# Kernel optimization log

Measured on AMD Instinct MI355X. Metric: run time of the kernel, lower is better.

The kernel has to match this reference:

```python
import jax, jax.numpy as jnp
import numpy as np

N = 50000
E = 640000
H = 128

def setup_inputs() -> dict:
    key = jax.random.key(0)
    ks = jax.random.split(key, 12)
    def lin(kw, fan_in, fan_out):
        # torch nn.Linear default init: U(-1/sqrt(fan_in), 1/sqrt(fan_in))
        lim = 1.0 / np.sqrt(fan_in)
        return jax.random.uniform(kw, (fan_in, fan_out), jnp.float32, -lim, lim)
    def bias(kb, fan_in, fan_out):
        lim = 1.0 / np.sqrt(fan_in)
        return jax.random.uniform(kb, (fan_out,), jnp.float32, -lim, lim)
    return {
        "x": jax.random.normal(ks[0], (N, H), jnp.float32),
        "pos": jax.random.normal(ks[1], (N, 3), jnp.float32),
        "edge_index": jax.random.randint(ks[2], (2, E), 0, N, jnp.int64),
        "msg_w1": lin(ks[3], 2 * H + 1, H), "msg_b1": bias(ks[4], 2 * H + 1, H),
        "msg_w2": lin(ks[5], H, H),         "msg_b2": bias(ks[6], H, H),
        "upd_w1": lin(ks[7], 2 * H, H),     "upd_b1": bias(ks[8], 2 * H, H),
        "upd_w2": lin(ks[9], H, H),         "upd_b2": bias(ks[10], H, H),
    }

def reference(x, pos, edge_index, msg_w1, msg_b1, msg_w2, msg_b2,
              upd_w1, upd_b1, upd_w2, upd_b2):
    send, rec = edge_index[0], edge_index[1]
    # pairwise distance per edge: [E]
    dist = jnp.linalg.norm(pos[send] - pos[rec], axis=1)
    # per-edge state: [E, 2H+1]
    state = jnp.concatenate([x[send], x[rec], dist[:, None]], axis=1)
    # message MLP: Linear -> SiLU -> Linear -> SiLU
    h = jax.nn.silu(state @ msg_w1 + msg_b1)
    message = jax.nn.silu(h @ msg_w2 + msg_b2)  # [E, H]
    # scatter-add into receiving nodes: [N, H]
    aggr = jax.ops.segment_sum(message, rec, num_segments=x.shape[0])
    # update MLP: Linear -> SiLU -> Linear
    u = jax.nn.silu(jnp.concatenate([x, aggr], axis=1) @ upd_w1 + upd_b1)
    update = u @ upd_w2 + upd_b2
    return update
```

## Files before the change

kernel.cpp:

```cpp
#include <hip/hip_runtime.h>
#include <math.h>

#define H 128

typedef unsigned short u16;
typedef unsigned int u32;
typedef __attribute__((ext_vector_type(4))) u32 u32x4;
typedef __attribute__((ext_vector_type(8))) __bf16 bf16x8;
typedef __attribute__((ext_vector_type(4))) float f32x4;
typedef __attribute__((ext_vector_type(16))) float f32x16;

union Frag { u32x4 u; bf16x8 b; };

__device__ __forceinline__ u32 pack2(float lo, float hi) {
    union { __bf16 b[2]; u32 u; } v;
    v.b[0] = (__bf16)lo; v.b[1] = (__bf16)hi;
    return v.u;
}
__device__ __forceinline__ float bflo(u32 w) {
    union { u32 i; float f; } v; v.i = w << 16; return v.f;
}
__device__ __forceinline__ float bfhi(u32 w) {
    union { u32 i; float f; } v; v.i = w & 0xffff0000u; return v.f;
}
__device__ __forceinline__ float silu(float v) {
    float e = __expf(-v);
    return v * __builtin_amdgcn_rcpf(1.0f + e);
}
__device__ __forceinline__ bf16x8 f8frag(float4 lo, float4 hi) {
    Frag f;
    f.u = (u32x4){pack2(lo.x, lo.y), pack2(lo.z, lo.w),
                  pack2(hi.x, hi.y), pack2(hi.z, hi.w)};
    return f.b;
}
__device__ __forceinline__ f32x16 mfma(bf16x8 a, bf16x8 b, f32x16 c) {
    return __builtin_amdgcn_mfma_f32_32x32x16_bf16(a, b, c, 0, 0, 0);
}
__device__ __forceinline__ f32x4 mfma16(bf16x8 a, bf16x8 b, f32x4 c) {
    return __builtin_amdgcn_mfma_f32_16x16x32_bf16(a, b, c, 0, 0, 0);
}
#define DPP_RADD(v, ctrl) \
    (v) += __int_as_float(__builtin_amdgcn_update_dpp(0, __float_as_int(v), (ctrl), 0xf, 0xf, 1))

__global__ void prep_kernel(const float* __restrict__ mw1, const float* __restrict__ mb1,
                            const float* __restrict__ mw2, const float* __restrict__ mb2,
                            const float* __restrict__ uw1, const float* __restrict__ ub1,
                            const float* __restrict__ uw2, const float* __restrict__ ub2,
                            u32* __restrict__ ws) {
    int t = blockIdx.x * blockDim.x + threadIdx.x;
    if (t >= 15936) return;
    if (t >= 15872) {
        int i = t - 15872;
        ws[63488 + i] = pack2(mw1[256 * H + 2 * i], mw1[256 * H + 2 * i + 1]);
        return;
    }
    if (t >= 13312) {
        int slot = t - 13312;
        int lane = slot & 63, fb = slot >> 6;
        int kb = fb >> 3, mt = fb & 7;
        int m = mt * 16 + (lane & 15);
        int quad = lane >> 4;
        u32 out[4];
        #pragma unroll
        for (int p = 0; p < 4; ++p) {
            float v[2];
            #pragma unroll
            for (int h = 0; h < 2; ++h) {
                int k = kb * 32 + quad * 8 + p * 2 + h;
                float val = 0.0f;
                if (k < 128)       val = mw2[(size_t)k * H + m];
                else if (k == 128) val = mb2[m];
                v[h] = val;
            }
            out[p] = pack2(v[0], v[1]);
        }
        u32* dst = ws + 53248 + (size_t)slot * 4;
        dst[0] = out[0]; dst[1] = out[1]; dst[2] = out[2]; dst[3] = out[3];
        return;
    }
    const float *W, *s0, *s1;
    int nK, slot, base;
    if (t < 4352)       { W = mw1; s0 = mw1 + 256 * H; s1 = mb1; nK = 256; slot = t;         base = 0;     }
    else if (t < 6656)  { W = mw2; s0 = mb2; s1 = nullptr;       nK = 128; slot = t - 4352;  base = 17408; }
    else if (t < 11008) { W = uw1; s0 = ub1; s1 = nullptr;       nK = 256; slot = t - 6656;  base = 26624; }
    else                { W = uw2; s0 = ub2; s1 = nullptr;       nK = 128; slot = t - 11008; base = 44032; }
    int lane = slot & 63, fb = slot >> 6;
    int ct, kb;
    if (nK == 256) { ct = fb / 17; kb = fb % 17; }
    else           { ct = fb / 9;  kb = fb % 9;  }
    int m = ct * 32 + (lane & 31);
    int q = lane >> 5;
    u32 out[4];
    #pragma unroll
    for (int p = 0; p < 4; ++p) {
        float v[2];
        #pragma unroll
        for (int h = 0; h < 2; ++h) {
            int k = kb * 16 + q * 8 + p * 2 + h;
            float val = 0.0f;
            if (k < nK)            val = W[(size_t)k * H + m];
            else if (k == nK)      val = s0 ? s0[m] : 0.0f;
            else if (k == nK + 1)  val = s1 ? s1[m] : 0.0f;
            v[h] = val;
        }
        out[p] = pack2(v[0], v[1]);
    }
    u32* dst = ws + base + (size_t)slot * 4;
    dst[0] = out[0]; dst[1] = out[1]; dst[2] = out[2]; dst[3] = out[3];
}

__global__ __launch_bounds__(256, 2) void pq_gemm(
    const float* __restrict__ x, const u32* __restrict__ mw1s,
    void* __restrict__ outp, int kbBase, int withBias, int packP, int N, int nIter)
{
    const int lane = threadIdx.x & 63;
    const int q = lane >> 5, el = lane & 31;
    const int gw  = blockIdx.x * 4 + (threadIdx.x >> 6);
    const int gws = gridDim.x * 4;

    for (int it = gw; it < nIter; it += gws) {
        const int nA = it * 32 + el;
        const int ncA = (nA < N) ? nA : (N - 1);
        const float* xA = x + (size_t)ncA * H;

        f32x16 acc[4];
        #pragma unroll
        for (int ct = 0; ct < 4; ++ct) acc[ct] = (f32x16)0.0f;

        #pragma unroll
        for (int kb = 0; kb < 8; ++kb) {
            const int f = kb * 16 + q * 8;
            bf16x8 bA = f8frag(*(const float4*)(xA + f), *(const float4*)(xA + f + 4));
            #pragma unroll
            for (int ct = 0; ct < 4; ++ct) {
                Frag a; a.u = *(const u32x4*)&mw1s[((size_t)(ct * 17 + kbBase + kb) * 64 + lane) * 4];
                acc[ct] = mfma(a.b, bA, acc[ct]);
            }
        }
        if (withBias) {
            Frag bp; bp.u = (u32x4){0, 0, 0, 0};
            if (q == 0) bp.u.x = pack2(0.0f, 1.0f);
            #pragma unroll
            for (int ct = 0; ct < 4; ++ct) {
                Frag a; a.u = *(const u32x4*)&mw1s[((size_t)(ct * 17 + 16) * 64 + lane) * 4];
                acc[ct] = mfma(a.b, bp.b, acc[ct]);
            }
        }
        if (nA < N) {
            if (packP) {
                u32* prow = (u32*)outp + (size_t)nA * 64;
                #pragma unroll
                for (int ct = 0; ct < 4; ++ct)
                    #pragma unroll
                    for (int g = 0; g < 4; ++g) {
                        u32 a = pack2(acc[ct][4*g + 0], acc[ct][4*g + 1]);
                        u32 b = pack2(acc[ct][4*g + 2], acc[ct][4*g + 3]);
                        *(uint2*)(prow + ct * 16 + 4 * g + 2 * q) = make_uint2(a, b);
                    }
            } else {
                float* orow = (float*)outp + (size_t)nA * H;
                #pragma unroll
                for (int ct = 0; ct < 4; ++ct)
                    #pragma unroll
                    for (int g = 0; g < 4; ++g) {
                        float4 v = { acc[ct][4*g + 0], acc[ct][4*g + 1],
                                     acc[ct][4*g + 2], acc[ct][4*g + 3] };
                        *(float4*)(orow + ct * 32 + 8 * g + 4 * q) = v;
                    }
            }
        }
    }
}

__global__ void bucket_fill(const float* __restrict__ pos, const int* __restrict__ ei,
                            int* __restrict__ deg, int2* __restrict__ bucket, int E)
{
    int e = blockIdx.x * blockDim.x + threadIdx.x;
    if (e >= E) return;
    const int s = ei[e];
    const int r = ei[E + e];
    const float dx = pos[s*3]   - pos[r*3];
    const float dy = pos[s*3+1] - pos[r*3+1];
    const float dz = pos[s*3+2] - pos[r*3+2];
    const float dist = sqrtf(dx*dx + dy*dy + dz*dz);
    int slot = atomicAdd(&deg[r], 1);
    if (slot < 64) bucket[(size_t)r * 64 + slot] = make_int2(s, __float_as_int(dist));
}

__global__ __launch_bounds__(256, 3) void aggregate_kernel(
    const u32* __restrict__ Pbf, const u32* __restrict__ Qbf,
    const u32* __restrict__ wdp, const u32* __restrict__ ws16,
    const float* __restrict__ mb2,
    const int* __restrict__ deg, const int2* __restrict__ bucket,
    float* __restrict__ out, int N)
{
    __shared__ u32x4 af[2048];
    __shared__ float b2s[128];
    __shared__ u32x4 wds[16];
    for (int i = threadIdx.x; i < 2048; i += 256) af[i] = ((const u32x4*)ws16)[i];
    for (int i = threadIdx.x; i < 128; i += 256) b2s[i] = mb2[i];
    if (threadIdx.x < 16) wds[threadIdx.x] = ((const u32x4*)wdp)[threadIdx.x];
    __syncthreads();

    const int lane = threadIdx.x & 63;
    const int quad = lane >> 4, col = lane & 15;

    const int gw  = blockIdx.x * 4 + (threadIdx.x >> 6);
    const int gws = gridDim.x * 4;

    for (int n = gw; n < N; n += gws) {
        int dn = deg[n]; dn = (dn > 64) ? 64 : dn;
        const int nt = (dn + 15) >> 4;
        const u32x4* Qrow = (const u32x4*)(Qbf + (size_t)n * 64);

        f32x4 sum[8];
        #pragma unroll
        for (int mt = 0; mt < 8; ++mt) sum[mt] = (f32x4){0.f, 0.f, 0.f, 0.f};

        for (int t = 0; t < nt; ++t) {
            const int eIdx = t * 16 + col;
            const bool valid = eIdx < dn;
            const int eC = valid ? eIdx : (dn - 1);
            const int2 rec = bucket[(size_t)n * 64 + eC];
            const u32x4* Prow = (const u32x4*)(Pbf + (size_t)rec.x * 64);
            const float dist = __int_as_float(rec.y);

            f32x4 acc[8];
            #pragma unroll
            for (int mt = 0; mt < 8; ++mt)
                acc[mt] = *(const f32x4*)&b2s[mt * 16 + quad * 4];

            #pragma unroll 2
            for (int kb = 0; kb < 4; ++kb) {
                const u32x4 pc = Prow[kb * 4 + quad];
                const u32x4 qc = Qrow[kb * 4 + quad];
                const u32x4 wc = wds[kb * 4 + quad];
                const float v0 = silu(bflo(pc.x) + bflo(qc.x) + dist * bflo(wc.x));
                const float v1 = silu(bfhi(pc.x) + bfhi(qc.x) + dist * bfhi(wc.x));
                const float v2 = silu(bflo(pc.y) + bflo(qc.y) + dist * bflo(wc.y));
                const float v3 = silu(bfhi(pc.y) + bfhi(qc.y) + dist * bfhi(wc.y));
                const float v4 = silu(bflo(pc.z) + bflo(qc.z) + dist * bflo(wc.z));
                const float v5 = silu(bfhi(pc.z) + bfhi(qc.z) + dist * bfhi(wc.z));
                const float v6 = silu(bflo(pc.w) + bflo(qc.w) + dist * bflo(wc.w));
                const float v7 = silu(bfhi(pc.w) + bfhi(qc.w) + dist * bfhi(wc.w));
                Frag bf;
                bf.u = (u32x4){pack2(v0, v1), pack2(v2, v3), pack2(v4, v5), pack2(v6, v7)};
                if (!valid) bf.u = (u32x4){0, 0, 0, 0};
                #pragma unroll
                for (int mt = 0; mt < 8; ++mt) {
                    Frag a; a.u = af[(kb * 8 + mt) * 64 + lane];
                    acc[mt] = mfma16(a.b, bf.b, acc[mt]);
                }
            }
            #pragma unroll
            for (int mt = 0; mt < 8; ++mt) {
                sum[mt][0] += valid ? silu(acc[mt][0]) : 0.0f;
                sum[mt][1] += valid ? silu(acc[mt][1]) : 0.0f;
                sum[mt][2] += valid ? silu(acc[mt][2]) : 0.0f;
                sum[mt][3] += valid ? silu(acc[mt][3]) : 0.0f;
            }
        }

        #pragma unroll
        for (int mt = 0; mt < 8; ++mt)
            #pragma unroll
            for (int r = 0; r < 4; ++r) {
                float v = sum[mt][r];
                DPP_RADD(v, 0x128);
                DPP_RADD(v, 0x124);
                DPP_RADD(v, 0x122);
                DPP_RADD(v, 0x121);
                sum[mt][r] = v;
            }
        if (col == 0) {
            float* orow = out + (size_t)n * H;
            #pragma unroll
            for (int mt = 0; mt < 8; ++mt) {
                float4 v = { sum[mt][0], sum[mt][1], sum[mt][2], sum[mt][3] };
                *(float4*)(orow + mt * 16 + quad * 4) = v;
            }
        }
    }
}

__global__ __launch_bounds__(256, 2) void edge_mfma(
    const float* __restrict__ x, const float* __restrict__ pos,
    const int* __restrict__ ei, const u32* __restrict__ ws,
    float* __restrict__ aggr, int E, int nIter)
{
    __shared__ u32 lds[16384];
    {
        const u32x4* src = (const u32x4*)ws;
        u32x4* dst = (u32x4*)lds;
        for (int i = threadIdx.x; i < 4096; i += 256) {
            int ln = i & 63, fb = i >> 6, ct = fb >> 4, kb = fb & 15;
            dst[i] = src[(ct * 17 + kb) * 64 + ln];
        }
    }
    __syncthreads();
    const u32* wsl1 = ws;
    const u32* wsl2 = ws + 17408;

    const int lane = threadIdx.x & 63;
    const int q = lane >> 5, el = lane & 31;
    const int gw  = blockIdx.x * 4 + (threadIdx.x >> 6);
    const int gws = gridDim.x * 4;

    for (int it = gw; it < nIter; it += gws) {
        const int e0 = it * 64;
        const int sA = ei[e0 + el],      rA = ei[E + e0 + el];
        const int sB = ei[e0 + 32 + el], rB = ei[E + e0 + 32 + el];
        float dA, dB;
        {
            float ax = pos[sA*3] - pos[rA*3], ay = pos[sA*3+1] - pos[rA*3+1], az = pos[sA*3+2] - pos[rA*3+2];
            dA = sqrtf(ax*ax + ay*ay + az*az);
            float bx = pos[sB*3] - pos[rB*3], by = pos[sB*3+1] - pos[rB*3+1], bz = pos[sB*3+2] - pos[rB*3+2];
            dB = sqrtf(bx*bx + by*by + bz*bz);
        }
        const float* xsA = x + (size_t)sA * H; const float* xrA = x + (size_t)rA * H;
        const float* xsB = x + (size_t)sB * H; const float* xrB = x + (size_t)rB * H;

        f32x16 acc[2][4];
        #pragma unroll
        for (int s = 0; s < 2; ++s)
            #pragma unroll
            for (int ct = 0; ct < 4; ++ct) acc[s][ct] = (f32x16)0.0f;

        #pragma unroll
        for (int kb = 0; kb < 16; ++kb) {
            const int f = kb * 16 + q * 8;
            const float* pA = (f < H) ? (xsA + f) : (xrA + f - H);
            const float* pB = (f < H) ? (xsB + f) : (xrB + f - H);
            bf16x8 bA = f8frag(*(const float4*)pA, *(const float4*)(pA + 4));
            bf16x8 bB = f8frag(*(const float4*)pB, *(const float4*)(pB + 4));
            #pragma unroll
            for (int ct = 0; ct < 4; ++ct) {
                Frag a; a.u = *(const u32x4*)&lds[((ct * 16 + kb) * 64 + lane) * 4];
                acc[0][ct] = mfma(a.b, bA, acc[0][ct]);
                acc[1][ct] = mfma(a.b, bB, acc[1][ct]);
            }
        }
        {
            Frag bA, bB;
            bA.u = (u32x4){0,0,0,0}; bB.u = (u32x4){0,0,0,0};
            if (q == 0) { bA.u.x = pack2(dA, 1.0f); bB.u.x = pack2(dB, 1.0f); }
            #pragma unroll
            for (int ct = 0; ct < 4; ++ct) {
                Frag a; a.u = *(const u32x4*)&wsl1[((size_t)(ct * 17 + 16) * 64 + lane) * 4];
                acc[0][ct] = mfma(a.b, bA.b, acc[0][ct]);
                acc[1][ct] = mfma(a.b, bB.b, acc[1][ct]);
            }
        }

        #pragma unroll
        for (int s = 0; s < 2; ++s) {
            const int ridx = s ? rB : rA;
            u32 hp[4][4][2];
            #pragma unroll
            for (int ct = 0; ct < 4; ++ct)
                #pragma unroll
                for (int g = 0; g < 4; ++g) {
                    float v0 = silu(acc[s][ct][4*g + 0]);
                    float v1 = silu(acc[s][ct][4*g + 1]);
                    float v2 = silu(acc[s][ct][4*g + 2]);
                    float v3 = silu(acc[s][ct][4*g + 3]);
                    hp[ct][g][0] = pack2(v0, v1);
                    hp[ct][g][1] = pack2(v2, v3);
                }

            f32x16 acc2[4];
            #pragma unroll
            for (int ct = 0; ct < 4; ++ct) acc2[ct] = (f32x16)0.0f;

            #pragma unroll
            for (int kb2 = 0; kb2 < 8; ++kb2) {
                const int om = 2 * kb2 + q;
                const int op = 2 * kb2 + 1 - q;
                u32 sv0 = hp[op >> 2][op & 3][0];
                u32 sv1 = hp[op >> 2][op & 3][1];
                u32 r0 = (u32)__shfl((int)sv0, lane ^ 32);
                u32 r1 = (u32)__shfl((int)sv1, lane ^ 32);
                u32 w0 = hp[om >> 2][om & 3][0];
                u32 w1v = hp[om >> 2][om & 3][1];
                Frag bf;
                if (q == 0) bf.u = (u32x4){w0, w1v, r0, r1};
                else        bf.u = (u32x4){r0, r1, w0, w1v};
                #pragma unroll
                for (int ct2 = 0; ct2 < 4; ++ct2) {
                    Frag a; a.u = *(const u32x4*)&wsl2[((size_t)(ct2 * 9 + kb2) * 64 + lane) * 4];
                    acc2[ct2] = mfma(a.b, bf.b, acc2[ct2]);
                }
            }
            {
                Frag bf; bf.u = (u32x4){0,0,0,0};
                if (q == 0) bf.u.x = 0x00003F80u;
                #pragma unroll
                for (int ct2 = 0; ct2 < 4; ++ct2) {
                    Frag a; a.u = *(const u32x4*)&wsl2[((size_t)(ct2 * 9 + 8) * 64 + lane) * 4];
                    acc2[ct2] = mfma(a.b, bf.b, acc2[ct2]);
                }
            }
            float* arow = aggr + (size_t)ridx * H;
            #pragma unroll
            for (int ct2 = 0; ct2 < 4; ++ct2)
                #pragma unroll
                for (int r = 0; r < 16; ++r) {
                    int m = ct2 * 32 + (r & 3) + 8 * (r >> 2) + 4 * q;
                    atomicAdd(arow + m, silu(acc2[ct2][r]));
                }
        }
    }
}

__global__ __launch_bounds__(256, 2) void node_mfma(
    const float* __restrict__ x, float* __restrict__ buf,
    const u32* __restrict__ ws, int N, int nIter)
{
    __shared__ u32 lds[16384];
    const u32* wsl1 = ws + 26624;
    const u32* wsl2 = ws + 44032;
    {
        const u32x4* src = (const u32x4*)wsl1;
        u32x4* dst = (u32x4*)lds;
        for (int i = threadIdx.x; i < 4096; i += 256) {
            int ln = i & 63, fb = i >> 6, ct = fb >> 4, kb = fb & 15;
            dst[i] = src[(ct * 17 + kb) * 64 + ln];
        }
    }
    __syncthreads();

    const int lane = threadIdx.x & 63;
    const int q = lane >> 5, el = lane & 31;
    const int gw  = blockIdx.x * 4 + (threadIdx.x >> 6);
    const int gws = gridDim.x * 4;

    for (int it = gw; it < nIter; it += gws) {
        const int nA = it * 32 + el;
        const int ncA = (nA < N) ? nA : (N - 1);
        const float* xA = x + (size_t)ncA * H;
        const float* gA = buf + (size_t)ncA * H;

        f32x16 acc[4];
        #pragma unroll
        for (int ct = 0; ct < 4; ++ct) acc[ct] = (f32x16)0.0f;

        #pragma unroll
        for (int kb = 0; kb < 16; ++kb) {
            const int f = kb * 16 + q * 8;
            const float* pA = (f < H) ? (xA + f) : (gA + f - H);
            bf16x8 bA = f8frag(*(const float4*)pA, *(const float4*)(pA + 4));
            #pragma unroll
            for (int ct = 0; ct < 4; ++ct) {
                Frag a; a.u = *(const u32x4*)&lds[((ct * 16 + kb) * 64 + lane) * 4];
                acc[ct] = mfma(a.b, bA, acc[ct]);
            }
        }
        {
            Frag bp; bp.u = (u32x4){0,0,0,0};
            if (q == 0) bp.u.x = 0x00003F80u;
            #pragma unroll
            for (int ct = 0; ct < 4; ++ct) {
                Frag a; a.u = *(const u32x4*)&wsl1[((size_t)(ct * 17 + 16) * 64 + lane) * 4];
                acc[ct] = mfma(a.b, bp.b, acc[ct]);
            }
        }

        u32 hp[4][4][2];
        #pragma unroll
        for (int ct = 0; ct < 4; ++ct)
            #pragma unroll
            for (int g = 0; g < 4; ++g) {
                float v0 = silu(acc[ct][4*g + 0]);
                float v1 = silu(acc[ct][4*g + 1]);
                float v2 = silu(acc[ct][4*g + 2]);
                float v3 = silu(acc[ct][4*g + 3]);
                hp[ct][g][0] = pack2(v0, v1);
                hp[ct][g][1] = pack2(v2, v3);
            }

        f32x16 acc2[4];
        #pragma unroll
        for (int ct = 0; ct < 4; ++ct) acc2[ct] = (f32x16)0.0f;

        #pragma unroll
        for (int kb2 = 0; kb2 < 8; ++kb2) {
            const int om = 2 * kb2 + q;
            const int op = 2 * kb2 + 1 - q;
            u32 sv0 = hp[op >> 2][op & 3][0];
            u32 sv1 = hp[op >> 2][op & 3][1];
            u32 r0 = (u32)__shfl((int)sv0, lane ^ 32);
            u32 r1 = (u32)__shfl((int)sv1, lane ^ 32);
            u32 w0 = hp[om >> 2][om & 3][0];
            u32 w1v = hp[om >> 2][om & 3][1];
            Frag bf;
            if (q == 0) bf.u = (u32x4){w0, w1v, r0, r1};
            else        bf.u = (u32x4){r0, r1, w0, w1v};
            #pragma unroll
            for (int ct2 = 0; ct2 < 4; ++ct2) {
                Frag a; a.u = *(const u32x4*)&wsl2[((size_t)(ct2 * 9 + kb2) * 64 + lane) * 4];
                acc2[ct2] = mfma(a.b, bf.b, acc2[ct2]);
            }
        }
        {
            Frag bf; bf.u = (u32x4){0,0,0,0};
            if (q == 0) bf.u.x = 0x00003F80u;
            #pragma unroll
            for (int ct2 = 0; ct2 < 4; ++ct2) {
                Frag a; a.u = *(const u32x4*)&wsl2[((size_t)(ct2 * 9 + 8) * 64 + lane) * 4];
                acc2[ct2] = mfma(a.b, bf.b, acc2[ct2]);
            }
        }
        if (nA < N) {
            float* orow = buf + (size_t)nA * H;
            #pragma unroll
            for (int ct2 = 0; ct2 < 4; ++ct2)
                #pragma unroll
                for (int g = 0; g < 4; ++g) {
                    float4 v = { acc2[ct2][4*g + 0], acc2[ct2][4*g + 1],
                                 acc2[ct2][4*g + 2], acc2[ct2][4*g + 3] };
                    *(float4*)(orow + ct2 * 32 + 8 * g + 4 * q) = v;
                }
        }
    }
}

extern "C" void kernel_launch(void* const* d_in, const int* in_sizes, int n_in,
                              void* d_out, int out_size, void* d_ws, size_t ws_size,
                              hipStream_t stream) {
    const float* x    = (const float*)d_in[0];
    const float* pos  = (const float*)d_in[1];
    const int*   ei   = (const int*)d_in[2];
    const float* mw1  = (const float*)d_in[3];
    const float* mb1  = (const float*)d_in[4];
    const float* mw2  = (const float*)d_in[5];
    const float* mb2  = (const float*)d_in[6];
    const float* uw1  = (const float*)d_in[7];
    const float* ub1  = (const float*)d_in[8];
    const float* uw2  = (const float*)d_in[9];
    const float* ub2  = (const float*)d_in[10];

    const int N = in_sizes[0] / H;
    const int E = in_sizes[2] / 2;

    const size_t FRAGS = 53248 + 10240 + 64;
    const size_t PO = FRAGS;
    const size_t QO = PO + (size_t)N * 64;
    const size_t DG = QO + (size_t)N * 64;
    const size_t BK = DG + (size_t)N;
    const size_t ENDu = BK + (size_t)N * 128;
    const size_t need_bytes = ENDu * 4;

    u32* ws = (u32*)d_ws;
    prep_kernel<<<63, 256, 0, stream>>>(mw1, mb1, mw2, mb2, uw1, ub1, uw2, ub2, ws);

    float* buf = (float*)d_out;
    const int nIter32 = (N + 31) / 32;

    if (ws_size >= need_bytes) {
        u32*   Pb   = ws + PO;
        u32*   Qb   = ws + QO;
        int*   deg  = (int*)(ws + DG);
        int2*  bkt  = (int2*)(ws + BK);

        pq_gemm<<<512, 256, 0, stream>>>(x, ws, Pb, 0, 0, 1, N, nIter32);
        pq_gemm<<<512, 256, 0, stream>>>(x, ws, Qb, 8, 1, 1, N, nIter32);

        hipMemsetAsync(deg, 0, (size_t)N * sizeof(int), stream);
        bucket_fill<<<(E + 255) / 256, 256, 0, stream>>>(pos, ei, deg, bkt, E);

        aggregate_kernel<<<768, 256, 0, stream>>>(Pb, Qb, ws + 63488, ws + 53248,
                                                  mb2, deg, bkt, buf, N);
        node_mfma<<<512, 256, 0, stream>>>(x, buf, ws, N, nIter32);
    } else {
        hipMemsetAsync(buf, 0, (size_t)N * H * sizeof(float), stream);
        edge_mfma<<<512, 256, 0, stream>>>(x, pos, ei, ws, buf, E, E / 64);
        node_mfma<<<512, 256, 0, stream>>>(x, buf, ws, N, nIter32);
    }
}
```

Measured before the change: 401.2 us.

## Merge P/Q GEMMs and bucket fill into one heterogeneous front kernel

```diff
diff --git a/kernel.cpp b/kernel.cpp
--- a/kernel.cpp
+++ b/kernel.cpp
@@ -109,82 +109,78 @@
     dst[0] = out[0]; dst[1] = out[1]; dst[2] = out[2]; dst[3] = out[3];
 }
 
-__global__ __launch_bounds__(256, 2) void pq_gemm(
+__global__ __launch_bounds__(256, 2) void front_kernel(
     const float* __restrict__ x, const u32* __restrict__ mw1s,
-    void* __restrict__ outp, int kbBase, int withBias, int packP, int N, int nIter)
+    u32* __restrict__ Pb, u32* __restrict__ Qb,
+    const float* __restrict__ pos, const int* __restrict__ ei,
+    int* __restrict__ deg, int2* __restrict__ bucket,
+    int N, int E, int nIter, int PQB, int BKB)
 {
-    const int lane = threadIdx.x & 63;
-    const int q = lane >> 5, el = lane & 31;
-    const int gw  = blockIdx.x * 4 + (threadIdx.x >> 6);
-    const int gws = gridDim.x * 4;
-
-    for (int it = gw; it < nIter; it += gws) {
-        const int nA = it * 32 + el;
-        const int ncA = (nA < N) ? nA : (N - 1);
-        const float* xA = x + (size_t)ncA * H;
-
-        f32x16 acc[4];
-        #pragma unroll
-        for (int ct = 0; ct < 4; ++ct) acc[ct] = (f32x16)0.0f;
-
-        #pragma unroll
-        for (int kb = 0; kb < 8; ++kb) {
-            const int f = kb * 16 + q * 8;
-            bf16x8 bA = f8frag(*(const float4*)(xA + f), *(const float4*)(xA + f + 4));
-            #pragma unroll
-            for (int ct = 0; ct < 4; ++ct) {
-                Frag a; a.u = *(const u32x4*)&mw1s[((size_t)(ct * 17 + kbBase + kb) * 64 + lane) * 4];
-                acc[ct] = mfma(a.b, bA, acc[ct]);
-            }
-        }
-        if (withBias) {
-            Frag bp; bp.u = (u32x4){0, 0, 0, 0};
-            if (q == 0) bp.u.x = pack2(0.0f, 1.0f);
-            #pragma unroll
-            for (int ct = 0; ct < 4; ++ct) {
-                Frag a; a.u = *(const u32x4*)&mw1s[((size_t)(ct * 17 + 16) * 64 + lane) * 4];
-                acc[ct] = mfma(a.b, bp.b, acc[ct]);
-            }
-        }
-        if (nA < N) {
-            if (packP) {
-                u32* prow = (u32*)outp + (size_t)nA * 64;
+    const int b = blockIdx.x;
+    if (b < 2 * PQB) {
+        const int isQ = (b >= PQB);
+        const int bb = isQ ? (b - PQB) : b;
+        const int kbBase = isQ ? 8 : 0;
+        u32* outb = isQ ? Qb : Pb;
+
+        const int lane = threadIdx.x & 63;
+        const int q = lane >> 5, el = lane & 31;
+        const int gw  = bb * 4 + (threadIdx.x >> 6);
+        const int gws = PQB * 4;
+
+        for (int it = gw; it < nIter; it += gws) {
+            const int nA = it * 32 + el;
+            const int ncA = (nA < N) ? nA : (N - 1);
+            const float* xA = x + (size_t)ncA * H;
+
+            f32x16 acc[4];
+            #pragma unroll
+            for (int ct = 0; ct < 4; ++ct) acc[ct] = (f32x16)0.0f;
+
+            #pragma unroll
+            for (int kb = 0; kb < 8; ++kb) {
+                const int f = kb * 16 + q * 8;
+                bf16x8 bA = f8frag(*(const float4*)(xA + f), *(const float4*)(xA + f + 4));
+                #pragma unroll
+                for (int ct = 0; ct < 4; ++ct) {
+                    Frag a; a.u = *(const u32x4*)&mw1s[((size_t)(ct * 17 + kbBase + kb) * 64 + lane) * 4];
+                    acc[ct] = mfma(a.b, bA, acc[ct]);
+                }
+            }
+            if (isQ) {
+                Frag bp; bp.u = (u32x4){0, 0, 0, 0};
+                if (q == 0) bp.u.x = pack2(0.0f, 1.0f);
+                #pragma unroll
+                for (int ct = 0; ct < 4; ++ct) {
+                    Frag a; a.u = *(const u32x4*)&mw1s[((size_t)(ct * 17 + 16) * 64 + lane) * 4];
+                    acc[ct] = mfma(a.b, bp.b, acc[ct]);
+                }
+            }
+            if (nA < N) {
+                u32* prow = outb + (size_t)nA * 64;
                 #pragma unroll
                 for (int ct = 0; ct < 4; ++ct)
                     #pragma unroll
                     for (int g = 0; g < 4; ++g) {
                         u32 a = pack2(acc[ct][4*g + 0], acc[ct][4*g + 1]);
-                        u32 b = pack2(acc[ct][4*g + 2], acc[ct][4*g + 3]);
-                        *(uint2*)(prow + ct * 16 + 4 * g + 2 * q) = make_uint2(a, b);
+                        u32 bb2 = pack2(acc[ct][4*g + 2], acc[ct][4*g + 3]);
+                        *(uint2*)(prow + ct * 16 + 4 * g + 2 * q) = make_uint2(a, bb2);
                     }
-            } else {
-                float* orow = (float*)outp + (size_t)nA * H;
-                #pragma unroll
-                for (int ct = 0; ct < 4; ++ct)
-                    #pragma unroll
-                    for (int g = 0; g < 4; ++g) {
-                        float4 v = { acc[ct][4*g + 0], acc[ct][4*g + 1],
-                                     acc[ct][4*g + 2], acc[ct][4*g + 3] };
-                        *(float4*)(orow + ct * 32 + 8 * g + 4 * q) = v;
-                    }
-            }
-        }
-    }
-}
-
-__global__ void bucket_fill(const float* __restrict__ pos, const int* __restrict__ ei,
-                            int* __restrict__ deg, int2* __restrict__ bucket, int E)
-{
-    int e = blockIdx.x * blockDim.x + threadIdx.x;
-    if (e >= E) return;
-    const int s = ei[e];
-    const int r = ei[E + e];
-    const float dx = pos[s*3]   - pos[r*3];
-    const float dy = pos[s*3+1] - pos[r*3+1];
-    const float dz = pos[s*3+2] - pos[r*3+2];
-    const float dist = sqrtf(dx*dx + dy*dy + dz*dz);
-    int slot = atomicAdd(&deg[r], 1);
-    if (slot < 64) bucket[(size_t)r * 64 + slot] = make_int2(s, __float_as_int(dist));
+            }
+        }
+    } else {
+        const int bb = b - 2 * PQB;
+        for (int e = bb * 256 + (int)threadIdx.x; e < E; e += BKB * 256) {
+            const int s = ei[e];
+            const int r = ei[E + e];
+            const float dx = pos[s*3]   - pos[r*3];
+            const float dy = pos[s*3+1] - pos[r*3+1];
+            const float dz = pos[s*3+2] - pos[r*3+2];
+            const float dist = sqrtf(dx*dx + dy*dy + dz*dz);
+            int slot = atomicAdd(&deg[r], 1);
+            if (slot < 64) bucket[(size_t)r * 64 + slot] = make_int2(s, __float_as_int(dist));
+        }
+    }
 }
 
 __global__ __launch_bounds__(256, 3) void aggregate_kernel(
@@ -562,11 +558,12 @@
         int*   deg  = (int*)(ws + DG);
         int2*  bkt  = (int2*)(ws + BK);
 
-        pq_gemm<<<512, 256, 0, stream>>>(x, ws, Pb, 0, 0, 1, N, nIter32);
-        pq_gemm<<<512, 256, 0, stream>>>(x, ws, Qb, 8, 1, 1, N, nIter32);
-
         hipMemsetAsync(deg, 0, (size_t)N * sizeof(int), stream);
-        bucket_fill<<<(E + 255) / 256, 256, 0, stream>>>(pos, ei, deg, bkt, E);
+
+        const int PQB = 392;
+        const int BKB = 640;
+        front_kernel<<<2 * PQB + BKB, 256, 0, stream>>>(
+            x, ws, Pb, Qb, pos, ei, deg, bkt, N, E, nIter32, PQB, BKB);
 
         aggregate_kernel<<<768, 256, 0, stream>>>(Pb, Qb, ws + 63488, ws + 53248,
                                                   mb2, deg, bkt, buf, N);
```

Measured after the change: 381.1 us. -5.0%, faster.
